# Performance work log

Measured on AMD Instinct MI355X. Metric: run time of the kernel, lower is better.

Reference implementation:

```python
import jax, jax.numpy as jnp
import numpy as np

B, N, T, K = 2048, 4096, 8192, 4
N_STATES = 3  # Potts states; small so max==min happens with real probability


def setup_inputs() -> dict:
    key = jax.random.key(0)
    k1, k2, k3 = jax.random.split(key, 3)
    # Potts variable states, stored as float32 (matches torch module which eq-compares raw x values)
    x = jax.random.randint(k1, (B, N), 0, N_STATES).astype(jnp.float32)
    coeffs = jax.random.normal(k2, (T,), dtype=jnp.float32)
    idx = jax.random.randint(k3, (T, K), 0, N, dtype=jnp.int32)
    return {"x": x, "coeffs": coeffs, "idx": idx}


def reference(x, coeffs, idx):
    # Vectorized form of: sum_t v_t * (max(x[..., key_t]) == min(x[..., key_t]))
    g = x[..., idx]                      # [B, T, K] gather of clique members
    eq = (jnp.max(g, axis=-1) == jnp.min(g, axis=-1)).astype(x.dtype)  # [B, T]
    return jnp.einsum('bt,t->b', eq, coeffs)  # [B]
```

## Files before the change

kernel.cpp:

```cpp
#include <hip/hip_runtime.h>


#define NN 4096
#define TT 8192
#define G 8
#define THREADS 512
#define TPT (TT / THREADS)

typedef unsigned long long u64;
typedef unsigned int u32;
typedef unsigned short u16;

__device__ __forceinline__ u32 code2(float f) {
    return (__float_as_uint(f) >> 29) & 3u;
}

__global__ __launch_bounds__(THREADS) void potts_kernel(
    const float* __restrict__ x,
    const float* __restrict__ coeffs,
    const int*   __restrict__ idx,
    float*       __restrict__ out)
{
    __shared__ u16 xs[NN];
    __shared__ float red[THREADS / 64][G];

    const int tid = threadIdx.x;
    const int b0  = blockIdx.x * G;

    int4  ii[TPT];
    float cf[TPT];
    #pragma unroll
    for (int i = 0; i < TPT; ++i) {
        const int t = tid + i * THREADS;
        ii[i] = *reinterpret_cast<const int4*>(idx + 4 * t);
        cf[i] = coeffs[t];
    }

    #pragma unroll
    for (int k = 0; k < NN / 4 / THREADS; ++k) {
        const int c  = tid + k * THREADS;
        const int n0 = c * 4;
        u64 v = 0;
        #pragma unroll
        for (int g = 0; g < G; ++g) {
            const float4 f =
                *reinterpret_cast<const float4*>(x + (size_t)(b0 + g) * NN + n0);
            v |= (u64)(code2(f.x) << (2 * g));
            v |= (u64)(code2(f.y) << (2 * g)) << 16;
            v |= (u64)(code2(f.z) << (2 * g)) << 32;
            v |= (u64)(code2(f.w) << (2 * g)) << 48;
        }
        reinterpret_cast<u64*>(xs)[c] = v;
    }
    __syncthreads();

    float acc[G];
    #pragma unroll
    for (int g = 0; g < G; ++g) acc[g] = 0.f;

    #pragma unroll
    for (int i = 0; i < TPT; ++i) {
        const u32 a = xs[ii[i].x];
        const u32 b = xs[ii[i].y];
        const u32 c = xs[ii[i].z];
        const u32 d = xs[ii[i].w];
        const u32 diff = (a ^ b) | (a ^ c) | (a ^ d);
        const u32 m = diff | (diff >> 1);
        const float cv = cf[i];
        #pragma unroll
        for (int g = 0; g < G; ++g)
            acc[g] += ((m >> (2 * g)) & 1u) ? 0.f : cv;
    }

    #pragma unroll
    for (int g = 0; g < G; ++g) {
        float v = acc[g];
        #pragma unroll
        for (int off = 32; off > 0; off >>= 1) v += __shfl_down(v, off, 64);
        if ((tid & 63) == 0) red[tid >> 6][g] = v;
    }
    __syncthreads();

    if (tid < G) {
        float s = 0.f;
        #pragma unroll
        for (int w = 0; w < THREADS / 64; ++w) s += red[w][tid];
        out[b0 + tid] = s;
    }
}

extern "C" void kernel_launch(void* const* d_in, const int* in_sizes, int n_in,
                              void* d_out, int out_size, void* d_ws, size_t ws_size,
                              hipStream_t stream) {
    const float* x      = (const float*)d_in[0];
    const float* coeffs = (const float*)d_in[1];
    const int*   idx    = (const int*)d_in[2];

    float* out = (float*)d_out;

    const int Bn   = in_sizes[0] / NN;
    const int grid = Bn / G;

    potts_kernel<<<grid, THREADS, 0, stream>>>(x, coeffs, idx, out);
}
```

Before: 14.25 us.

## Split packing into separate kernel and parallelize gather over term slices

Packs the 2-bit Potts codes for 16 batch rows per u32 in a dedicated pack kernel that writes to workspace. A second kernel loads the packed row group into shared memory and handles one quarter of the terms. Partial sums go to the output with atomicAdd after a memset. This widens each lane's bit-parallel work to 16 rows and raises grid parallelism. In exchange it adds two extra launches, a workspace round-trip, and atomics that make the summation order nondeterministic.

```diff
diff --git a/kernel.cpp b/kernel.cpp
--- a/kernel.cpp
+++ b/kernel.cpp
@@ -2,55 +2,69 @@
 
 
 #define NN 4096
+#define BB 2048
 #define TT 8192
-#define G 8
-#define THREADS 512
-#define TPT (TT / THREADS)
+#define G 16
+#define NBG (BB / G)
+#define PKT 256
+#define PK_CHUNK 1024
+#define PK_GRID (NBG * (NN / PK_CHUNK))
+#define GT 512
+#define TS 4
+#define G_GRID (NBG * TS)
+#define TPT (TT / TS / GT)
 
-typedef unsigned long long u64;
 typedef unsigned int u32;
-typedef unsigned short u16;
 
 __device__ __forceinline__ u32 code2(float f) {
     return (__float_as_uint(f) >> 29) & 3u;
 }
 
-__global__ __launch_bounds__(THREADS) void potts_kernel(
-    const float* __restrict__ x,
-    const float* __restrict__ coeffs,
-    const int*   __restrict__ idx,
-    float*       __restrict__ out)
+__global__ __launch_bounds__(PKT) void pack_kernel(
+    const float* __restrict__ x, u32* __restrict__ pk)
 {
-    __shared__ u16 xs[NN];
-    __shared__ float red[THREADS / 64][G];
+    const int bg = blockIdx.x >> 2;
+    const int ch = blockIdx.x & 3;
+    const int n0 = ch * PK_CHUNK + threadIdx.x * 4;
+    u32 w0 = 0, w1 = 0, w2 = 0, w3 = 0;
+    #pragma unroll
+    for (int g = 0; g < G; ++g) {
+        const float4 f =
+            *reinterpret_cast<const float4*>(x + (size_t)(bg * G + g) * NN + n0);
+        w0 |= code2(f.x) << (2 * g);
+        w1 |= code2(f.y) << (2 * g);
+        w2 |= code2(f.z) << (2 * g);
+        w3 |= code2(f.w) << (2 * g);
+    }
+    *reinterpret_cast<uint4*>(pk + (size_t)bg * NN + n0) = make_uint4(w0, w1, w2, w3);
+}
+
+__global__ __launch_bounds__(GT) void gather_kernel(
+    const u32* __restrict__ pk, const float* __restrict__ coeffs,
+    const int* __restrict__ idx, float* __restrict__ out)
+{
+    __shared__ u32 xs[NN];
+    __shared__ float red[GT / 64][G];
 
     const int tid = threadIdx.x;
-    const int b0  = blockIdx.x * G;
+    const int bg  = blockIdx.x >> 2;
+    const int th  = blockIdx.x & 3;
 
     int4  ii[TPT];
     float cf[TPT];
+    const int tbase = th * (TT / TS);
     #pragma unroll
     for (int i = 0; i < TPT; ++i) {
-        const int t = tid + i * THREADS;
+        const int t = tbase + tid + i * GT;
         ii[i] = *reinterpret_cast<const int4*>(idx + 4 * t);
         cf[i] = coeffs[t];
     }
 
     #pragma unroll
-    for (int k = 0; k < NN / 4 / THREADS; ++k) {
-        const int c  = tid + k * THREADS;
-        const int n0 = c * 4;
-        u64 v = 0;
-        #pragma unroll
-        for (int g = 0; g < G; ++g) {
-            const float4 f =
-                *reinterpret_cast<const float4*>(x + (size_t)(b0 + g) * NN + n0);
-            v |= (u64)(code2(f.x) << (2 * g));
-            v |= (u64)(code2(f.y) << (2 * g)) << 16;
-            v |= (u64)(code2(f.z) << (2 * g)) << 32;
-            v |= (u64)(code2(f.w) << (2 * g)) << 48;
-        }
-        reinterpret_cast<u64*>(xs)[c] = v;
+    for (int k = 0; k < NN / 4 / GT; ++k) {
+        const int c = tid + k * GT;
+        reinterpret_cast<uint4*>(xs)[c] =
+            reinterpret_cast<const uint4*>(pk + (size_t)bg * NN)[c];
     }
     __syncthreads();
 
@@ -84,8 +98,8 @@
     if (tid < G) {
         float s = 0.f;
         #pragma unroll
-        for (int w = 0; w < THREADS / 64; ++w) s += red[w][tid];
-        out[b0 + tid] = s;
+        for (int w = 0; w < GT / 64; ++w) s += red[w][tid];
+        atomicAdd(&out[bg * G + tid], s);
     }
 }
 
@@ -97,9 +111,9 @@
     const int*   idx    = (const int*)d_in[2];
 
     float* out = (float*)d_out;
+    u32*   pk  = (u32*)d_ws;
 
-    const int Bn   = in_sizes[0] / NN;
-    const int grid = Bn / G;
-
-    potts_kernel<<<grid, THREADS, 0, stream>>>(x, coeffs, idx, out);
+    hipMemsetAsync(d_out, 0, (size_t)out_size * sizeof(float), stream);
+    pack_kernel<<<PK_GRID, PKT, 0, stream>>>(x, pk);
+    gather_kernel<<<G_GRID, GT, 0, stream>>>(pk, coeffs, idx, out);
 }
```

Result: slower. 25.16 us (+76.6%).
